# Optimization experiments

Measured on AMD Instinct MI355X. Metric: run time of the kernel, lower is better.

The kernel has to match this reference:

```python
import jax, jax.numpy as jnp
import numpy as np

N_LAYERS = 2  # params.gcn_layers
R, N, D = 8, 4096, 128  # total_rel, total_ent, emb_dim


def setup_inputs() -> dict:
    key = jax.random.key(0)
    k1, k2, k3 = jax.random.split(key, 3)
    adj_mat = jax.random.uniform(k1, (R, N, N), dtype=jnp.float32)
    ent_emb = jax.random.uniform(k2, (N, D), dtype=jnp.float32)   # buffer (torch.rand)
    rel_trans = jax.random.uniform(k3, (R, D, D), dtype=jnp.float32)  # learned param
    return {"adj_mat": adj_mat, "ent_emb": ent_emb, "rel_trans": rel_trans}


def reference(adj_mat, ent_emb, rel_trans):
    # Faithful to GCN.forward: per layer,
    #   emb_acc[r] = adj[r] @ stop_grad(emb)          (R, N, D)
    #   tmp[r]     = (rel_trans[r] @ emb_acc[r].T).T  (R, N, D)
    #   emb        = relu(mean_r(tmp))                (N, D)
    emb = ent_emb
    for _ in range(N_LAYERS):
        agg = jnp.einsum('rnm,md->rnd', adj_mat, jax.lax.stop_gradient(emb))
        tmp = jnp.einsum('rde,rne->rnd', rel_trans, agg)
        emb = jax.nn.relu(jnp.mean(tmp, axis=0))
    return emb
```

## Files before the change

kernel.cpp:

```cpp
#include <hip/hip_runtime.h>

#define R_ 8
#define N_ 4096
#define D_ 128
#define BM 64
#define KSPLIT 2

typedef __attribute__((ext_vector_type(8))) short bf16x8;
typedef __attribute__((ext_vector_type(4))) float f32x4;

__device__ __forceinline__ unsigned short f2bf(float f) {
  unsigned int u = __builtin_bit_cast(unsigned int, f);
  u += 0x7FFFu + ((u >> 16) & 1u);
  return (unsigned short)(u >> 16);
}
__device__ __forceinline__ unsigned int pk4fp8(float a, float b, float c, float d) {
  int v = __builtin_amdgcn_cvt_pk_fp8_f32(a, b, 0, false);
  v = __builtin_amdgcn_cvt_pk_fp8_f32(c, d, v, true);
  return (unsigned int)v;
}

__device__ __forceinline__ void gld16(const void* g, void* l) {
  using GP = const __attribute__((address_space(1))) unsigned int*;
  using LP = __attribute__((address_space(3))) unsigned int*;
  __builtin_amdgcn_global_load_lds((GP)g, (LP)l, 16, 0, 0);
}

__global__ void k_init(const float* __restrict__ emb, const float* __restrict__ rel,
                       unsigned char* __restrict__ embT8a, unsigned short* __restrict__ relb) {
  int b = blockIdx.x;
  if (b < 256) {
    int gt = b * 256 + threadIdx.x;
    int C = gt >> 6, l = gt & 63;
    int d = (C & 7) * 16 + (l & 15);
    int k = (C >> 3) * 32 + (l >> 4) * 8;
    float v[8];
#pragma unroll
    for (int i = 0; i < 8; ++i)
      v[i] = emb[(size_t)(k + i) * D_ + d];
    uint2 pk;
    pk.x = pk4fp8(v[0], v[1], v[2], v[3]);
    pk.y = pk4fp8(v[4], v[5], v[6], v[7]);
    *(uint2*)(embT8a + ((size_t)C * 64 + l) * 8) = pk;
  } else {
    int i = (b - 256) * 256 + threadIdx.x;
    relb[i] = f2bf(rel[i]);
  }
}

__global__ __launch_bounds__(256, 3) void gcn_gemm1(
    const float* __restrict__ adj,
    const unsigned char* __restrict__ embT8a,
    unsigned char* __restrict__ adjf8,
    unsigned short* __restrict__ agg_p)
{
  __shared__ float         As[BM * 128];
  __shared__ unsigned char B8[16384];

  const int tid  = threadIdx.x;
  const int lane = tid & 63;
  const int w    = tid >> 6;
  const int wr = w >> 1, wc = w & 1;
  const int fr  = lane & 15;
  const int g   = lane >> 4;
  const int cr4 = g * 4;

  const int ntile = blockIdx.x;
  const int r     = blockIdx.y;
  const int z     = blockIdx.z;
  const int row0  = ntile * BM;
  const int k0    = z * (N_ / KSPLIT);
  const size_t tbase = (size_t)(r * 64 + ntile) * 262144;

  const float* gAr = adj + ((size_t)r * N_ + row0) * N_ + k0;

  f32x4 acc[2][4];
#pragma unroll
  for (int m = 0; m < 2; ++m)
#pragma unroll
    for (int n = 0; n < 4; ++n)
      acc[m][n] = (f32x4){0.f, 0.f, 0.f, 0.f};

  for (int t = 0; t < 16; ++t) {
    const int ko = t * 128;
#pragma unroll
    for (int i = 0; i < 8; ++i) {
      const int rowbase = w * 16 + i * 2;
      const int ra   = rowbase + (lane >> 5);
      const int slot = (lane & 31) ^ (ra & 15);
      gld16(gAr + (size_t)ra * N_ + ko + slot * 4, As + rowbase * 128);
    }
    {
      const unsigned char* src = embT8a + (size_t)(z * 64 + t * 4) * 4096;
#pragma unroll
      for (int i = 0; i < 4; ++i) {
        const int c = i * 4 + w;
        gld16(src + (size_t)c * 1024 + (size_t)lane * 16, B8 + c * 1024);
      }
    }
    __syncthreads();

#pragma unroll
    for (int kk = 0; kk < 4; ++kk) {
      unsigned long long av[2];
#pragma unroll
      for (int m = 0; m < 2; ++m) {
        const int row = wr * 32 + m * 16 + fr;
        const int s0  = kk * 8 + g * 2;
        f32x4 a0 = *(const f32x4*)&As[row * 128 + (((s0    ) ^ (row & 15)) * 4)];
        f32x4 a1 = *(const f32x4*)&As[row * 128 + (((s0 + 1) ^ (row & 15)) * 4)];
        unsigned int lo = pk4fp8(a0.x, a0.y, a0.z, a0.w);
        unsigned int hi = pk4fp8(a1.x, a1.y, a1.z, a1.w);
        av[m] = (unsigned long long)lo | ((unsigned long long)hi << 32);
      }
      if (wc == 0) {
        const int G = z * 64 + t * 4 + kk;
        unsigned char* p = adjf8 + tbase + (size_t)(G * 2 + wr) * 1024 + (size_t)lane * 8;
        *(unsigned long long*)p         = av[0];
        *(unsigned long long*)(p + 512) = av[1];
      }
#pragma unroll
      for (int n = 0; n < 4; ++n) {
        const int DB = wc * 4 + n;
        const long bv = *(const long*)&B8[((kk * 8 + DB) * 64 + lane) * 8];
#pragma unroll
        for (int m = 0; m < 2; ++m)
          acc[m][n] = __builtin_amdgcn_mfma_f32_16x16x32_fp8_fp8((long)av[m], bv, acc[m][n], 0, 0, 0);
      }
    }
    __syncthreads();
  }

  unsigned short* gO = agg_p + (((size_t)z * R_ + r) * N_ + row0) * D_;
#pragma unroll
  for (int m = 0; m < 2; ++m)
#pragma unroll
    for (int n = 0; n < 4; ++n)
#pragma unroll
      for (int j = 0; j < 4; ++j) {
        int rl = wr * 32 + m * 16 + cr4 + j;
        int cl = wc * 64 + n * 16 + fr;
        gO[(size_t)rl * D_ + cl] = f2bf(acc[m][n][j]);
      }
}

__global__ __launch_bounds__(256, 4) void gcn_gemm2(
    const unsigned char* __restrict__ adjf8,
    const unsigned char* __restrict__ embT8t,
    unsigned short* __restrict__ agg_p)
{
  __shared__ unsigned char A8[4096];
  __shared__ unsigned char B8[8192];

  const int tid  = threadIdx.x;
  const int lane = tid & 63;
  const int w    = tid >> 6;
  const int fr   = lane & 15;
  const int cr4  = (lane >> 4) * 4;

  const int ntile = blockIdx.x;
  const int r     = blockIdx.y;
  const int z     = blockIdx.z;
  const int row0  = ntile * BM;
  const size_t tbase = (size_t)(r * 64 + ntile) * 262144;

  f32x4 acc[8];
#pragma unroll
  for (int n = 0; n < 8; ++n)
    acc[n] = (f32x4){0.f, 0.f, 0.f, 0.f};

  for (int t = 0; t < 32; ++t) {
    const int G0 = z * 64 + t * 2;
    gld16(adjf8 + tbase + (size_t)G0 * 2048 + (size_t)w * 1024 + (size_t)lane * 16,
          A8 + w * 1024);
#pragma unroll
    for (int i = 0; i < 2; ++i) {
      const int c = i * 4 + w;
      gld16(embT8t + (size_t)G0 * 4096 + (size_t)c * 1024 + (size_t)lane * 16,
            B8 + c * 1024);
    }
    __syncthreads();

#pragma unroll
    for (int kk = 0; kk < 2; ++kk) {
      const long av = *(const long*)&A8[(((kk * 2 + (w >> 1)) * 2 + (w & 1)) * 64 + lane) * 8];
#pragma unroll
      for (int n = 0; n < 8; ++n) {
        const long bv = *(const long*)&B8[((kk * 8 + n) * 64 + lane) * 8];
        acc[n] = __builtin_amdgcn_mfma_f32_16x16x32_fp8_fp8(av, bv, acc[n], 0, 0, 0);
      }
    }
    __syncthreads();
  }

  unsigned short* gO = agg_p + (((size_t)z * R_ + r) * N_ + row0) * D_;
#pragma unroll
  for (int n = 0; n < 8; ++n)
#pragma unroll
    for (int j = 0; j < 4; ++j) {
      int rl = w * 16 + cr4 + j;
      int cl = n * 16 + fr;
      gO[(size_t)rl * D_ + cl] = f2bf(acc[n][j]);
    }
}

__global__ __launch_bounds__(256) void gcn_pass2(
    const unsigned short* __restrict__ agg_p,
    const unsigned short* __restrict__ relb,
    float* __restrict__ out,
    unsigned char* __restrict__ embT8t,
    int write_out, int write_embT)
{
  const int tid  = threadIdx.x;
  const int lane = tid & 63;
  const int w    = tid >> 6;
  const int n0   = blockIdx.x * 16;
  const int col0 = w * 32;
  const int fr   = lane & 15;
  const int e8   = (lane >> 4) * 8;
  const int cr4  = (lane >> 4) * 4;

  f32x4 tacc[2];
  tacc[0] = (f32x4){0.f, 0.f, 0.f, 0.f};
  tacc[1] = (f32x4){0.f, 0.f, 0.f, 0.f};

  for (int r = 0; r < R_; ++r) {
    bf16x8 a[2][4], b[2][4];
#pragma unroll
    for (int zz = 0; zz < 2; ++zz)
#pragma unroll
      for (int kk = 0; kk < 4; ++kk)
        a[zz][kk] = *(const bf16x8*)&agg_p[(((size_t)zz * R_ + r) * N_ + n0 + fr) * D_ + kk * 32 + e8];
#pragma unroll
    for (int n = 0; n < 2; ++n)
#pragma unroll
      for (int kk = 0; kk < 4; ++kk)
        b[n][kk] = *(const bf16x8*)&relb[(size_t)r * D_ * D_ + (col0 + n * 16 + fr) * D_ + kk * 32 + e8];
#pragma unroll
    for (int n = 0; n < 2; ++n)
#pragma unroll
      for (int kk = 0; kk < 4; ++kk)
#pragma unroll
        for (int zz = 0; zz < 2; ++zz)
          tacc[n] = __builtin_amdgcn_mfma_f32_16x16x32_bf16(a[zz][kk], b[n][kk], tacc[n], 0, 0, 0);
  }

#pragma unroll
  for (int n = 0; n < 2; ++n) {
    if (write_out) {
#pragma unroll
      for (int j = 0; j < 4; ++j) {
        int row = n0 + cr4 + j;
        int col = col0 + n * 16 + fr;
        float v = tacc[n][j] * 8192.f;
        out[(size_t)row * D_ + col] = v > 0.f ? v : 0.f;
      }
    }
    if (write_embT) {
      const float s = 0.125f * 1.52587890625e-05f;
      float v[4];
#pragma unroll
      for (int j = 0; j < 4; ++j) {
        float x = tacc[n][j];
        v[j] = (x > 0.f ? x : 0.f) * s;
      }
      unsigned int pk = pk4fp8(v[0], v[1], v[2], v[3]);
      const int G   = n0 >> 5;
      const int gfr = ((n0 & 31) + cr4) >> 3;
      const int h   = (cr4 >> 2) & 1;
      const int DB  = w * 2 + n;
      *(unsigned int*)(embT8t + (size_t)(G * 8 + DB) * 512 + (fr + gfr * 16) * 8 + h * 4) = pk;
    }
  }
}

extern "C" void kernel_launch(void* const* d_in, const int* in_sizes, int n_in,
                              void* d_out, int out_size, void* d_ws, size_t ws_size,
                              hipStream_t stream) {
  const float* adj = (const float*)d_in[0];
  const float* emb = (const float*)d_in[1];
  const float* rel = (const float*)d_in[2];
  float* out = (float*)d_out;

  unsigned short* relb   = (unsigned short*)d_ws;
  unsigned short* agg_p  = relb + (size_t)R_ * D_ * D_;
  unsigned char*  embT8a = (unsigned char*)(agg_p + (size_t)2 * R_ * N_ * D_);
  unsigned char*  embT8t = embT8a + (size_t)512 * 1024;
  unsigned char*  adjf8  = embT8t + (size_t)512 * 1024;

  k_init<<<768, 256, 0, stream>>>(emb, rel, embT8a, relb);

  dim3 grid(N_ / BM, R_, KSPLIT);
  gcn_gemm1<<<grid, 256, 0, stream>>>(adj, embT8a, adjf8, agg_p);
  gcn_pass2<<<N_ / 16, 256, 0, stream>>>(agg_p, relb, out, embT8t, 0, 1);
  gcn_gemm2<<<grid, 256, 0, stream>>>(adjf8, embT8t, agg_p);
  gcn_pass2<<<N_ / 16, 256, 0, stream>>>(agg_p, relb, out, embT8t, 1, 0);
}
```

Before: 216.9 us.

## Double-buffer adj tiles in LDS and load fp8 emb operand directly to registers

Converts the gemm1 main loop to a two-stage pipeline. The next adj fp32 tile is prefetched into a second LDS buffer while the current one is converted and multiplied, using explicit vmcnt waits and raw barriers. The fp8 embedding B fragments are now read from global memory straight into registers instead of being staged through LDS. The larger LDS footprint lowers the occupancy hint from 3 to 2 blocks per CU, and the hand-tuned waitcnt counts depend on how loads and stores are counted.

```diff
diff --git a/kernel.cpp b/kernel.cpp
--- a/kernel.cpp
+++ b/kernel.cpp
@@ -48,14 +48,13 @@
   }
 }
 
-__global__ __launch_bounds__(256, 3) void gcn_gemm1(
+__global__ __launch_bounds__(256, 2) void gcn_gemm1(
     const float* __restrict__ adj,
     const unsigned char* __restrict__ embT8a,
     unsigned char* __restrict__ adjf8,
     unsigned short* __restrict__ agg_p)
 {
-  __shared__ float         As[BM * 128];
-  __shared__ unsigned char B8[16384];
+  __shared__ float As[2][BM * 128];
 
   const int tid  = threadIdx.x;
   const int lane = tid & 63;
@@ -81,25 +80,40 @@
     for (int n = 0; n < 4; ++n)
       acc[m][n] = (f32x4){0.f, 0.f, 0.f, 0.f};
 
+#pragma unroll
+  for (int i = 0; i < 8; ++i) {
+    const int rowbase = w * 16 + i * 2;
+    const int ra   = rowbase + (lane >> 5);
+    const int slot = (lane & 31) ^ (ra & 15);
+    gld16(gAr + (size_t)ra * N_ + slot * 4, &As[0][rowbase * 128]);
+  }
+
   for (int t = 0; t < 16; ++t) {
-    const int ko = t * 128;
-#pragma unroll
-    for (int i = 0; i < 8; ++i) {
-      const int rowbase = w * 16 + i * 2;
-      const int ra   = rowbase + (lane >> 5);
-      const int slot = (lane & 31) ^ (ra & 15);
-      gld16(gAr + (size_t)ra * N_ + ko + slot * 4, As + rowbase * 128);
-    }
-    {
-      const unsigned char* src = embT8a + (size_t)(z * 64 + t * 4) * 4096;
-#pragma unroll
-      for (int i = 0; i < 4; ++i) {
-        const int c = i * 4 + w;
-        gld16(src + (size_t)c * 1024 + (size_t)lane * 16, B8 + c * 1024);
-      }
-    }
-    __syncthreads();
-
+    unsigned long long bv[4][4];
+#pragma unroll
+    for (int kk = 0; kk < 4; ++kk)
+#pragma unroll
+      for (int n = 0; n < 4; ++n)
+        bv[kk][n] = *(const unsigned long long*)
+            (embT8a + ((((size_t)(z * 64 + t * 4 + kk) * 8) + wc * 4 + n) * 64 + lane) * 8);
+
+    if (t + 1 < 16) {
+      const int ko = (t + 1) * 128;
+#pragma unroll
+      for (int i = 0; i < 8; ++i) {
+        const int rowbase = w * 16 + i * 2;
+        const int ra   = rowbase + (lane >> 5);
+        const int slot = (lane & 31) ^ (ra & 15);
+        gld16(gAr + (size_t)ra * N_ + ko + slot * 4, &As[(t + 1) & 1][rowbase * 128]);
+      }
+      asm volatile("s_waitcnt vmcnt(8)" ::: "memory");
+    } else {
+      asm volatile("s_waitcnt vmcnt(0)" ::: "memory");
+    }
+    __builtin_amdgcn_sched_barrier(0);
+    __builtin_amdgcn_s_barrier();
+
+    const float* Ab = As[t & 1];
 #pragma unroll
     for (int kk = 0; kk < 4; ++kk) {
       unsigned long long av[2];
@@ -107,8 +121,8 @@
       for (int m = 0; m < 2; ++m) {
         const int row = wr * 32 + m * 16 + fr;
         const int s0  = kk * 8 + g * 2;
-        f32x4 a0 = *(const f32x4*)&As[row * 128 + (((s0    ) ^ (row & 15)) * 4)];
-        f32x4 a1 = *(const f32x4*)&As[row * 128 + (((s0 + 1) ^ (row & 15)) * 4)];
+        f32x4 a0 = *(const f32x4*)&Ab[row * 128 + (((s0    ) ^ (row & 15)) * 4)];
+        f32x4 a1 = *(const f32x4*)&Ab[row * 128 + (((s0 + 1) ^ (row & 15)) * 4)];
         unsigned int lo = pk4fp8(a0.x, a0.y, a0.z, a0.w);
         unsigned int hi = pk4fp8(a1.x, a1.y, a1.z, a1.w);
         av[m] = (unsigned long long)lo | ((unsigned long long)hi << 32);
@@ -120,15 +134,13 @@
         *(unsigned long long*)(p + 512) = av[1];
       }
 #pragma unroll
-      for (int n = 0; n < 4; ++n) {
-        const int DB = wc * 4 + n;
-        const long bv = *(const long*)&B8[((kk * 8 + DB) * 64 + lane) * 8];
+      for (int n = 0; n < 4; ++n)
 #pragma unroll
         for (int m = 0; m < 2; ++m)
-          acc[m][n] = __builtin_amdgcn_mfma_f32_16x16x32_fp8_fp8((long)av[m], bv, acc[m][n], 0, 0, 0);
-      }
-    }
-    __syncthreads();
+          acc[m][n] = __builtin_amdgcn_mfma_f32_16x16x32_fp8_fp8(
+              (long)av[m], (long)bv[kk][n], acc[m][n], 0, 0, 0);
+    }
+    __builtin_amdgcn_s_barrier();
   }
 
   unsigned short* gO = agg_p + (((size_t)z * R_ + r) * N_ + row0) * D_;
```

New measurement: 219.8 us. No clear change (+1.3%).
